# Performance work log

Hardware: AMD Instinct MI355X
Metric: run time of the kernel (lower is better)

## Reference

```python
import jax, jax.numpy as jnp
import numpy as np

H = 4096      # num_patches (sequence length)
WS = 8        # window_size
SHIFT = 4     # shift_size
NH = 8        # num_heads
DIM = 512     # embedding dim
HD = DIM // NH
NW = H // WS  # windows per batch element
B = 16
LN_EPS = 1e-5


def _layer_norm(x, g, b):
    m = jnp.mean(x, axis=-1, keepdims=True)
    v = jnp.var(x, axis=-1, keepdims=True)
    return (x - m) * jax.lax.rsqrt(v + LN_EPS) * g + b


def _window_partition(x):
    # Faithful to the repo: reshape->permute(nW<->ws)->flatten, giving strided windows.
    Bx, N, C = x.shape
    return x.reshape(Bx, N // WS, WS, C).transpose(0, 2, 1, 3).reshape(-1, WS, C)


def _window_reverse(w, N, Bx):
    C = w.shape[-1]
    return w.reshape(Bx, N // WS, WS, C).transpose(0, 2, 1, 3).reshape(Bx, N, C)


def _attn_mask():
    # Built exactly as in __init__ (numpy, constant at trace time): (NW, WS, WS)
    m = np.zeros((1, H, 1), np.float32)
    m[:, :H - WS] = 0.0
    m[:, H - WS:H - SHIFT] = 1.0
    m[:, H - SHIFT:] = 2.0
    mw = m.reshape(1, NW, WS, 1).transpose(0, 2, 1, 3).reshape(-1, WS)  # (NW, WS)
    d = mw[:, None, :] - mw[:, :, None]
    return np.where(d != 0, np.float32(-100.0), np.float32(0.0))


def _forward(x, norm1_g, norm1_b, qkv_w, qkv_b, proj_w, proj_b,
             norm2_g, norm2_b, fc1_w, fc1_b, fc2_w, fc2_b):
    Bx = x.shape[0]
    shortcut = x
    xn = _layer_norm(x, norm1_g, norm1_b)
    xs = jnp.roll(xn, -SHIFT, axis=1)
    xw = _window_partition(xs)                       # (Bx*NW, WS, DIM)
    B_ = xw.shape[0]
    qkv = xw @ qkv_w.T + qkv_b                       # (B_, WS, 3*DIM)
    qkv = qkv.reshape(B_, WS, 3, NH, HD).transpose(2, 0, 3, 1, 4)
    q, k, v = qkv[0], qkv[1], qkv[2]                 # (B_, NH, WS, HD)
    attn = jnp.einsum('bhqd,bhkd->bhqk', q, k) * (HD ** -0.5)
    mask = jnp.asarray(_attn_mask())                 # (NW, WS, WS)
    attn = attn.reshape(B_ // NW, NW, NH, WS, WS) + mask[None, :, None]
    attn = jax.nn.softmax(attn.reshape(B_, NH, WS, WS), axis=-1)
    o = jnp.einsum('bhqk,bhkd->bqhd', attn, v).reshape(B_, WS, DIM)
    o = o @ proj_w.T + proj_b
    xr = _window_reverse(o, H, Bx)
    xr = jnp.roll(xr, SHIFT, axis=1)
    x1 = shortcut + xr
    h = _layer_norm(x1, norm2_g, norm2_b)
    h = jax.nn.gelu(h @ fc1_w.T + fc1_b, approximate=False)
    h = h @ fc2_w.T + fc2_b
    return x1 + h


def setup_inputs() -> dict:
    key = jax.random.key(0)
    ks = jax.random.split(key, 8)
    s = 0.02
    return {
        'x': jax.random.normal(ks[0], (B, H, DIM), jnp.float32),
        'norm1_g': jnp.ones((DIM,), jnp.float32),
        'norm1_b': jnp.zeros((DIM,), jnp.float32),
        'qkv_w': jax.random.normal(ks[1], (3 * DIM, DIM), jnp.float32) * s,
        'qkv_b': jnp.zeros((3 * DIM,), jnp.float32),
        'proj_w': jax.random.normal(ks[2], (DIM, DIM), jnp.float32) * s,
        'proj_b': jnp.zeros((DIM,), jnp.float32),
        'norm2_g': jnp.ones((DIM,), jnp.float32),
        'norm2_b': jnp.zeros((DIM,), jnp.float32),
        'fc1_w': jax.random.normal(ks[3], (4 * DIM, DIM), jnp.float32) * s,
        'fc1_b': jnp.zeros((4 * DIM,), jnp.float32),
        'fc2_w': jax.random.normal(ks[4], (DIM, 4 * DIM), jnp.float32) * s,
        'fc2_b': jnp.zeros((DIM,), jnp.float32),
    }


def reference(x, norm1_g, norm1_b, qkv_w, qkv_b, proj_w, proj_b,
              norm2_g, norm2_b, fc1_w, fc1_b, fc2_w, fc2_b):
    return _forward(x, norm1_g, norm1_b, qkv_w, qkv_b, proj_w, proj_b,
                    norm2_g, norm2_b, fc1_w, fc1_b, fc2_w, fc2_b)
```

## Files before the change

kernel.cpp:

```cpp
#include <hip/hip_runtime.h>
#include <hip/hip_bf16.h>
#include <math.h>

typedef unsigned short ushortT;
typedef __attribute__((ext_vector_type(8))) short short8;
typedef __attribute__((ext_vector_type(4))) short short4v;
typedef __attribute__((ext_vector_type(4))) float f32x4;
typedef __attribute__((ext_vector_type(4))) float float4v;

#define TOK 65536
#define NSEQ 4096
#define DIM 512

__device__ __forceinline__ float bf2f(ushortT u) {
  union { float f; unsigned int i; } v; v.i = ((unsigned int)u) << 16; return v.f;
}
__device__ __forceinline__ ushortT f2bf(float f) {
  union { float f; unsigned int i; } v; v.f = f;
  unsigned int r = v.i + 0x7fffu + ((v.i >> 16) & 1u);
  return (ushortT)(r >> 16);
}

__device__ __forceinline__ float fast_gelu(float x) {
  const float y = fabsf(x) * 0.70710678118654752f;
  const float t = __builtin_amdgcn_rcpf(__builtin_fmaf(0.3275911f, y, 1.f));
  float p = 1.061405429f;
  p = __builtin_fmaf(p, t, -1.453152027f);
  p = __builtin_fmaf(p, t, 1.421413741f);
  p = __builtin_fmaf(p, t, -0.284496736f);
  p = __builtin_fmaf(p, t, 0.254829592f);
  p = p * t;
  const float e = __builtin_amdgcn_exp2f(-y * y * 1.4426950408889634f);
  float erfv = __builtin_fmaf(-p, e, 1.f);
  erfv = copysignf(erfv, x);
  return 0.5f * x * (1.f + erfv);
}

#define GLOAD_LDS(gp, lp) __builtin_amdgcn_global_load_lds( \
    (const __attribute__((address_space(1))) unsigned int*)(gp), \
    (__attribute__((address_space(3))) unsigned int*)(lp), 16, 0, 0)

#define LGKM0 do { asm volatile("s_waitcnt lgkmcnt(0)" ::: "memory"); \
                   __builtin_amdgcn_sched_barrier(0); } while (0)
#define BAR __builtin_amdgcn_s_barrier()
#define VMC(n) asm volatile("s_waitcnt vmcnt(" #n ")" ::: "memory")
#define SB0 __builtin_amdgcn_sched_barrier(0)

__global__ void cvt_kernel(const float* __restrict__ in, ushortT* __restrict__ out, int n4) {
  int i = blockIdx.x * 256 + threadIdx.x;
  if (i >= n4) return;
  float4v v = *(const float4v*)(in + (size_t)i * 4);
  short4v o;
#pragma unroll
  for (int j = 0; j < 4; ++j) o[j] = (short)f2bf(v[j]);
  *(short4v*)(out + (size_t)i * 4) = o;
}

template <bool INBF>
__global__ __launch_bounds__(256)
void ln_kernel(const void* __restrict__ inp, const float* __restrict__ gw,
               const float* __restrict__ bw, ushortT* __restrict__ out)
{
  const int lane = threadIdx.x & 63;
  const size_t tok = (size_t)blockIdx.x * 4 + (threadIdx.x >> 6);
  const int col = lane * 8;
  float x[8];
  if constexpr (INBF) {
    short8 v = *(const short8*)((const ushortT*)inp + tok * DIM + col);
#pragma unroll
    for (int j = 0; j < 8; ++j) x[j] = bf2f((ushortT)v[j]);
  } else {
    const float* p = (const float*)inp + tok * DIM + col;
    float4v a = *(const float4v*)p, b = *(const float4v*)(p + 4);
#pragma unroll
    for (int j = 0; j < 4; ++j) { x[j] = a[j]; x[4 + j] = b[j]; }
  }
  float s = 0.f, ss = 0.f;
#pragma unroll
  for (int j = 0; j < 8; ++j) { s += x[j]; ss += x[j] * x[j]; }
#pragma unroll
  for (int off = 1; off < 64; off <<= 1) {
    s += __shfl_xor(s, off, 64);
    ss += __shfl_xor(ss, off, 64);
  }
  const float mean = s * (1.f / 512.f);
  const float var = ss * (1.f / 512.f) - mean * mean;
  const float rstd = rsqrtf(var + 1e-5f);
  float4v g1 = *(const float4v*)(gw + col), g2 = *(const float4v*)(gw + col + 4);
  float4v b1 = *(const float4v*)(bw + col), b2 = *(const float4v*)(bw + col + 4);
  short8 o;
#pragma unroll
  for (int j = 0; j < 4; ++j) {
    o[j]     = (short)f2bf((x[j]     - mean) * rstd * g1[j] + b1[j]);
    o[4 + j] = (short)f2bf((x[4 + j] - mean) * rstd * g2[j] + b2[j]);
  }
  *(short8*)(out + tok * DIM + col) = o;
}

#define MFMA_PHASE(MQ, NQ) \
  _Pragma("unroll") \
  for (int s_ = 0; s_ < 2; ++s_) \
    _Pragma("unroll") \
    for (int m_ = 0; m_ < 4; ++m_) \
      _Pragma("unroll") \
      for (int n_ = 0; n_ < 2; ++n_) \
        acc[(MQ) * 4 + m_][(NQ) * 2 + n_] = __builtin_amdgcn_mfma_f32_16x16x32_bf16( \
            Af[m_][s_], Bf[NQ][n_][s_], acc[(MQ) * 4 + m_][(NQ) * 2 + n_], 0, 0, 0)

#define STAGE_A(bufp, h, kt) do { \
    GLOAD_LDS(gA + (size_t)((h) * 128) * K + (size_t)(kt) * 64,     (bufp) + (h) * 8192 + w * 1024); \
    GLOAD_LDS(gA + (size_t)((h) * 128 + 8) * K + (size_t)(kt) * 64, (bufp) + (h) * 8192 + w * 1024 + 512); \
  } while (0)
#define STAGE_B(bufp, h, kt) do { \
    GLOAD_LDS(gB + (size_t)((h) * 128) * K + (size_t)(kt) * 64,     (bufp) + (h) * 8192 + w * 1024); \
    GLOAD_LDS(gB + (size_t)((h) * 128 + 8) * K + (size_t)(kt) * 64, (bufp) + (h) * 8192 + w * 1024 + 512); \
  } while (0)

template <int EPI>
__global__ __launch_bounds__(512, 2)
void gemm256(const ushortT* __restrict__ A, const ushortT* __restrict__ Bt,
             const float* __restrict__ bias, int M, int N, int K,
             ushortT* __restrict__ outb, float* __restrict__ outf,
             const float* __restrict__ resf, const ushortT* __restrict__ resb)
{
  __shared__ __align__(16) ushortT sm[65536];
  ushortT* const Ab0 = sm;
  ushortT* const Ab1 = sm + 16384;
  ushortT* const Bb0 = sm + 32768;
  ushortT* const Bb1 = sm + 49152;

  const int tid = threadIdx.x;
  const int w = tid >> 6, l = tid & 63;
  const int wr = w >> 2, wc = w & 3;

  const int nwg = gridDim.x * gridDim.y;
  int wg = blockIdx.y * gridDim.x + blockIdx.x;
  {
    const int q = nwg >> 3, r8 = nwg & 7;
    const int xc = wg & 7, yc = wg >> 3;
    wg = (xc < r8 ? xc * (q + 1) : r8 * (q + 1) + (xc - r8) * q) + yc;
  }
  const int nbn = N >> 8;
  const int mb = wg / nbn, nb = wg % nbn;
  const int m0 = mb << 8, n0 = nb << 8;
  const int NT = K >> 6;

  const ushortT* gA = A  + (size_t)(m0 + w * 16 + (l >> 3)) * K + (((l & 7) ^ (l >> 3)) << 3);
  const ushortT* gB = Bt + (size_t)(n0 + w * 16 + (l >> 3)) * K + (((l & 7) ^ (l >> 3)) << 3);

  const int rl = l & 15, ql = l >> 4;
  const int aoff = (wr * 128 + rl) * 64;
  const int boff = (wc * 64 + rl) * 64;
  const int cs0 = ((ql) ^ (l & 7)) << 3;
  const int cs1 = ((4 + ql) ^ (l & 7)) << 3;

  f32x4 acc[8][4];
  const f32x4 zero = {0.f, 0.f, 0.f, 0.f};
#pragma unroll
  for (int i = 0; i < 8; ++i)
#pragma unroll
    for (int j = 0; j < 4; ++j) acc[i][j] = zero;

  ushortT* Ac = Ab0; ushortT* An = Ab1;
  ushortT* Bc = Bb0; ushortT* Bn = Bb1;

  STAGE_A(Ac, 0, 0); STAGE_A(Ac, 1, 0); STAGE_B(Bc, 0, 0); STAGE_B(Bc, 1, 0);
  STAGE_A(An, 0, 1); STAGE_A(An, 1, 1); STAGE_B(Bn, 0, 1);
  VMC(6);
  BAR;

  short8 Af[4][2];
  short8 Bf[2][2][2];

  for (int t = 0; t < NT; ++t) {
#pragma unroll
    for (int m = 0; m < 4; ++m) {
      Af[m][0] = *(const short8*)(Ac + aoff + m * 1024 + cs0);
      Af[m][1] = *(const short8*)(Ac + aoff + m * 1024 + cs1);
    }
#pragma unroll
    for (int n = 0; n < 2; ++n) {
      Bf[0][n][0] = *(const short8*)(Bc + boff + n * 1024 + cs0);
      Bf[0][n][1] = *(const short8*)(Bc + boff + n * 1024 + cs1);
    }
    if (t + 1 < NT) STAGE_B(Bn, 1, t + 1);
    SB0;
    BAR; LGKM0;
    __builtin_amdgcn_s_setprio(1);
    MFMA_PHASE(0, 0);
    __builtin_amdgcn_s_setprio(0);
    BAR;
#pragma unroll
    for (int n = 0; n < 2; ++n) {
      Bf[1][n][0] = *(const short8*)(Bc + boff + (2 + n) * 1024 + cs0);
      Bf[1][n][1] = *(const short8*)(Bc + boff + (2 + n) * 1024 + cs1);
    }
    SB0;
    BAR; LGKM0;
    __builtin_amdgcn_s_setprio(1);
    MFMA_PHASE(0, 1);
    __builtin_amdgcn_s_setprio(0);
    BAR;
#pragma unroll
    for (int m = 0; m < 4; ++m) {
      Af[m][0] = *(const short8*)(Ac + aoff + (4 + m) * 1024 + cs0);
      Af[m][1] = *(const short8*)(Ac + aoff + (4 + m) * 1024 + cs1);
    }
    SB0;
    BAR; LGKM0;
    __builtin_amdgcn_s_setprio(1);
    MFMA_PHASE(1, 0);
    __builtin_amdgcn_s_setprio(0);
    BAR;
    SB0;
    if (t + 2 < NT) {
      STAGE_A(Ac, 0, t + 2); STAGE_A(Ac, 1, t + 2); STAGE_B(Bc, 0, t + 2);
      VMC(6);
    } else if (t + 1 < NT) {
      VMC(0);
    }
    __builtin_amdgcn_s_setprio(1);
    MFMA_PHASE(1, 1);
    __builtin_amdgcn_s_setprio(0);
    BAR;
    ushortT* tp;
    tp = Ac; Ac = An; An = tp;
    tp = Bc; Bc = Bn; Bn = tp;
  }

#pragma unroll
  for (int m = 0; m < 8; ++m) {
#pragma unroll
    for (int n = 0; n < 4; ++n) {
      const int col = n0 + wc * 64 + n * 16 + rl;
      const float bb = bias[col];
#pragma unroll
      for (int i = 0; i < 4; ++i) {
        const size_t row = (size_t)(m0 + wr * 128 + m * 16 + ql * 4 + i);
        float v = acc[m][n][i] + bb;
        if constexpr (EPI == 1) v += resf[row * (size_t)N + col];
        if constexpr (EPI == 2) v = fast_gelu(v);
        if constexpr (EPI == 3) {
          v += bf2f(resb[row * (size_t)N + col]);
          outf[row * (size_t)N + col] = v;
        } else {
          outb[row * (size_t)N + col] = f2bf(v);
        }
      }
    }
  }
}

__global__ __launch_bounds__(512)
void attn_kernel(const ushortT* __restrict__ qkv, ushortT* __restrict__ out)
{
  __shared__ __align__(16) ushortT sq[8][1544];
  const int wb = blockIdx.x;
  const int b  = wb >> 9;
  const int rr = wb & 511;
  const int w1 = rr >> 6;
  const int g  = rr & 63;
  const int tid = threadIdx.x;

#pragma unroll
  for (int c = 0; c < 3; ++c) {
    const int f = c * 512 + tid;
    const int i = f / 192;
    const int col = (f % 192) * 8;
    const int tin = (64 * g + 8 * i + w1 + 4) & (NSEQ - 1);
    const ushortT* src = qkv + ((size_t)b * NSEQ + tin) * 1536 + col;
    *(short8*)(&sq[i][col]) = *(const short8*)src;
  }
  __syncthreads();

  const int wave = tid >> 6, lane = tid & 63;
  const int h = wave;
  const int qi = lane >> 3, kj = lane & 7;

  float s = 0.f;
  const ushortT* qrow = &sq[qi][h * 64];
  const ushortT* krow = &sq[kj][512 + h * 64];
#pragma unroll
  for (int c = 0; c < 8; ++c) {
    short8 qa = *(const short8*)(qrow + c * 8);
    short8 ka = *(const short8*)(krow + c * 8);
#pragma unroll
    for (int j = 0; j < 8; ++j) s += bf2f((ushortT)qa[j]) * bf2f((ushortT)ka[j]);
  }
  s *= 0.125f;

  const int pq = 64 * g + 8 * qi + w1;
  const int pk = 64 * g + 8 * kj + w1;
  const int cq = (pq < 4088) ? 0 : (pq < 4092 ? 1 : 2);
  const int ck = (pk < 4088) ? 0 : (pk < 4092 ? 1 : 2);
  if (cq != ck) s -= 100.f;

  float mx = s;
  mx = fmaxf(mx, __shfl_xor(mx, 1, 64));
  mx = fmaxf(mx, __shfl_xor(mx, 2, 64));
  mx = fmaxf(mx, __shfl_xor(mx, 4, 64));
  const float e = expf(s - mx);
  float sum = e;
  sum += __shfl_xor(sum, 1, 64);
  sum += __shfl_xor(sum, 2, 64);
  sum += __shfl_xor(sum, 4, 64);
  const float p = e / sum;

  const int dc = lane & 7;
  float o[8];
#pragma unroll
  for (int j = 0; j < 8; ++j) o[j] = 0.f;
#pragma unroll
  for (int k2 = 0; k2 < 8; ++k2) {
    const float pk2 = __shfl(p, (lane & ~7) + k2, 64);
    short8 va = *(const short8*)(&sq[k2][1024 + h * 64 + dc * 8]);
#pragma unroll
    for (int j = 0; j < 8; ++j) o[j] += pk2 * bf2f((ushortT)va[j]);
  }

  const int tout = (512 * qi + 64 * w1 + g + 4) & (NSEQ - 1);
  short8 ov;
#pragma unroll
  for (int j = 0; j < 8; ++j) ov[j] = (short)f2bf(o[j]);
  *(short8*)(out + ((size_t)b * NSEQ + tout) * DIM + h * 64 + dc * 8) = ov;
}

extern "C" void kernel_launch(void* const* d_in, const int* in_sizes, int n_in,
                              void* d_out, int out_size, void* d_ws, size_t ws_size,
                              hipStream_t stream) {
  const float* x      = (const float*)d_in[0];
  const float* n1g    = (const float*)d_in[1];
  const float* n1b    = (const float*)d_in[2];
  const float* qkv_w  = (const float*)d_in[3];
  const float* qkv_b  = (const float*)d_in[4];
  const float* proj_w = (const float*)d_in[5];
  const float* proj_b = (const float*)d_in[6];
  const float* n2g    = (const float*)d_in[7];
  const float* n2b    = (const float*)d_in[8];
  const float* fc1_w  = (const float*)d_in[9];
  const float* fc1_b  = (const float*)d_in[10];
  const float* fc2_w  = (const float*)d_in[11];
  const float* fc2_b  = (const float*)d_in[12];
  float* out = (float*)d_out;

  size_t off = 0;
  char* ws = (char*)d_ws;
  auto alloc = [&](size_t b) { void* p = ws + off; off += (b + 255) & ~(size_t)255; return p; };

  ushortT* qkvw_b = (ushortT*)alloc((size_t)1536 * 512 * 2);
  ushortT* projw_b = (ushortT*)alloc((size_t)512 * 512 * 2);
  ushortT* fc1w_b = (ushortT*)alloc((size_t)2048 * 512 * 2);
  ushortT* fc2w_b = (ushortT*)alloc((size_t)512 * 2048 * 2);
  ushortT* bufA = (ushortT*)alloc((size_t)TOK * 512 * 2);
  ushortT* bufQ = (ushortT*)alloc((size_t)TOK * 1536 * 2);
  ushortT* x1 = bufQ;

  int nch = 1;
  while (nch < 16) {
    size_t need = (size_t)(TOK / nch) * 2048 * 2;
    if (off + need <= ws_size) break;
    nch <<= 1;
  }
  ushortT* h1 = (ushortT*)(ws + off);

  cvt_kernel<<<(1536 * 512 / 4 + 255) / 256, 256, 0, stream>>>(qkv_w, qkvw_b, 1536 * 512 / 4);
  cvt_kernel<<<(512 * 512 / 4 + 255) / 256, 256, 0, stream>>>(proj_w, projw_b, 512 * 512 / 4);
  cvt_kernel<<<(2048 * 512 / 4 + 255) / 256, 256, 0, stream>>>(fc1_w, fc1w_b, 2048 * 512 / 4);
  cvt_kernel<<<(512 * 2048 / 4 + 255) / 256, 256, 0, stream>>>(fc2_w, fc2w_b, 512 * 2048 / 4);

  ln_kernel<false><<<TOK / 4, 256, 0, stream>>>(x, n1g, n1b, bufA);

  gemm256<0><<<dim3(TOK / 256, 1536 / 256), 512, 0, stream>>>(
      bufA, qkvw_b, qkv_b, TOK, 1536, 512, bufQ, nullptr, nullptr, nullptr);

  attn_kernel<<<8192, 512, 0, stream>>>(bufQ, bufA);

  gemm256<1><<<dim3(TOK / 256, 512 / 256), 512, 0, stream>>>(
      bufA, projw_b, proj_b, TOK, 512, 512, x1, nullptr, x, nullptr);

  ln_kernel<true><<<TOK / 4, 256, 0, stream>>>(x1, n2g, n2b, bufA);

  const int tc = TOK / nch;
  for (int c = 0; c < nch; ++c) {
    const ushortT* hin = bufA + (size_t)c * tc * 512;
    gemm256<2><<<dim3(tc / 256, 2048 / 256), 512, 0, stream>>>(
        hin, fc1w_b, fc1_b, tc, 2048, 512, h1, nullptr, nullptr, nullptr);
    gemm256<3><<<dim3(tc / 256, 512 / 256), 512, 0, stream>>>(
        h1, fc2w_b, fc2_b, tc, 512, 2048, nullptr, out + (size_t)c * tc * 512,
        nullptr, x1 + (size_t)c * tc * 512);
  }
}
```

Baseline: 700.0 us.

## Restructure GEMM main loop to simple double-buffered prefetch with k-split fragment phases

Replaces the staggered two-tile-ahead staging scheme with a plain double buffer. The whole next k-tile is issued at the start of each iteration and waited on at the end. The MFMA phases are reorganised to split along the k-halves (cs0/cs1) with all four B fragments live, rather than splitting along N. This removes some barriers and register-held fragment arrays, which simplifies scheduling and lowers register pressure. In exchange, load latency is hidden by only one iteration of compute instead of the finer-grained interleaving.

```diff
diff --git a/kernel.cpp b/kernel.cpp
--- a/kernel.cpp
+++ b/kernel.cpp
@@ -97,23 +97,21 @@
   *(short8*)(out + tok * DIM + col) = o;
 }
 
-#define MFMA_PHASE(MQ, NQ) \
+#define MFMA_PHASE(MH) \
   _Pragma("unroll") \
-  for (int s_ = 0; s_ < 2; ++s_) \
+  for (int m_ = 0; m_ < 4; ++m_) \
     _Pragma("unroll") \
-    for (int m_ = 0; m_ < 4; ++m_) \
-      _Pragma("unroll") \
-      for (int n_ = 0; n_ < 2; ++n_) \
-        acc[(MQ) * 4 + m_][(NQ) * 2 + n_] = __builtin_amdgcn_mfma_f32_16x16x32_bf16( \
-            Af[m_][s_], Bf[NQ][n_][s_], acc[(MQ) * 4 + m_][(NQ) * 2 + n_], 0, 0, 0)
-
-#define STAGE_A(bufp, h, kt) do { \
-    GLOAD_LDS(gA + (size_t)((h) * 128) * K + (size_t)(kt) * 64,     (bufp) + (h) * 8192 + w * 1024); \
-    GLOAD_LDS(gA + (size_t)((h) * 128 + 8) * K + (size_t)(kt) * 64, (bufp) + (h) * 8192 + w * 1024 + 512); \
+    for (int n_ = 0; n_ < 4; ++n_) \
+      acc[(MH) * 4 + m_][n_] = __builtin_amdgcn_mfma_f32_16x16x32_bf16( \
+          Af[m_], Bf[n_], acc[(MH) * 4 + m_][n_], 0, 0, 0)
+
+#define STAGE_A2(bufp, h, gptr) do { \
+    GLOAD_LDS((gptr) + (size_t)((h) * 128) * K,     (bufp) + (h) * 8192 + w * 1024); \
+    GLOAD_LDS((gptr) + (size_t)((h) * 128 + 8) * K, (bufp) + (h) * 8192 + w * 1024 + 512); \
   } while (0)
-#define STAGE_B(bufp, h, kt) do { \
-    GLOAD_LDS(gB + (size_t)((h) * 128) * K + (size_t)(kt) * 64,     (bufp) + (h) * 8192 + w * 1024); \
-    GLOAD_LDS(gB + (size_t)((h) * 128 + 8) * K + (size_t)(kt) * 64, (bufp) + (h) * 8192 + w * 1024 + 512); \
+#define STAGE_B2(bufp, h, gptr) do { \
+    GLOAD_LDS((gptr) + (size_t)((h) * 128) * K,     (bufp) + (h) * 8192 + w * 1024); \
+    GLOAD_LDS((gptr) + (size_t)((h) * 128 + 8) * K, (bufp) + (h) * 8192 + w * 1024 + 512); \
   } while (0)
 
 template <int EPI>
@@ -164,68 +162,53 @@
   ushortT* Ac = Ab0; ushortT* An = Ab1;
   ushortT* Bc = Bb0; ushortT* Bn = Bb1;
 
-  STAGE_A(Ac, 0, 0); STAGE_A(Ac, 1, 0); STAGE_B(Bc, 0, 0); STAGE_B(Bc, 1, 0);
-  STAGE_A(An, 0, 1); STAGE_A(An, 1, 1); STAGE_B(Bn, 0, 1);
-  VMC(6);
+  STAGE_A2(Ac, 0, gA); STAGE_A2(Ac, 1, gA);
+  STAGE_B2(Bc, 0, gB); STAGE_B2(Bc, 1, gB);
+  VMC(0);
   BAR;
 
-  short8 Af[4][2];
-  short8 Bf[2][2][2];
+  short8 Af[4], Bf[4];
+  size_t koff = 64;
 
   for (int t = 0; t < NT; ++t) {
 #pragma unroll
-    for (int m = 0; m < 4; ++m) {
-      Af[m][0] = *(const short8*)(Ac + aoff + m * 1024 + cs0);
-      Af[m][1] = *(const short8*)(Ac + aoff + m * 1024 + cs1);
+    for (int m = 0; m < 4; ++m) Af[m] = *(const short8*)(Ac + aoff + m * 1024 + cs0);
+#pragma unroll
+    for (int n = 0; n < 4; ++n) Bf[n] = *(const short8*)(Bc + boff + n * 1024 + cs0);
+    if (t + 1 < NT) {
+      STAGE_A2(An, 0, gA + koff); STAGE_A2(An, 1, gA + koff);
+      STAGE_B2(Bn, 0, gB + koff); STAGE_B2(Bn, 1, gB + koff);
     }
-#pragma unroll
-    for (int n = 0; n < 2; ++n) {
-      Bf[0][n][0] = *(const short8*)(Bc + boff + n * 1024 + cs0);
-      Bf[0][n][1] = *(const short8*)(Bc + boff + n * 1024 + cs1);
-    }
-    if (t + 1 < NT) STAGE_B(Bn, 1, t + 1);
-    SB0;
-    BAR; LGKM0;
+    SB0; BAR; LGKM0;
     __builtin_amdgcn_s_setprio(1);
-    MFMA_PHASE(0, 0);
+    MFMA_PHASE(0);
     __builtin_amdgcn_s_setprio(0);
-    BAR;
-#pragma unroll
-    for (int n = 0; n < 2; ++n) {
-      Bf[1][n][0] = *(const short8*)(Bc + boff + (2 + n) * 1024 + cs0);
-      Bf[1][n][1] = *(const short8*)(Bc + boff + (2 + n) * 1024 + cs1);
-    }
-    SB0;
-    BAR; LGKM0;
+#pragma unroll
+    for (int m = 0; m < 4; ++m) Af[m] = *(const short8*)(Ac + aoff + (4 + m) * 1024 + cs0);
+    SB0; BAR; LGKM0;
     __builtin_amdgcn_s_setprio(1);
-    MFMA_PHASE(0, 1);
+    MFMA_PHASE(1);
     __builtin_amdgcn_s_setprio(0);
-    BAR;
-#pragma unroll
-    for (int m = 0; m < 4; ++m) {
-      Af[m][0] = *(const short8*)(Ac + aoff + (4 + m) * 1024 + cs0);
-      Af[m][1] = *(const short8*)(Ac + aoff + (4 + m) * 1024 + cs1);
-    }
-    SB0;
-    BAR; LGKM0;
+#pragma unroll
+    for (int m = 0; m < 4; ++m) Af[m] = *(const short8*)(Ac + aoff + m * 1024 + cs1);
+#pragma unroll
+    for (int n = 0; n < 4; ++n) Bf[n] = *(const short8*)(Bc + boff + n * 1024 + cs1);
+    SB0; BAR; LGKM0;
     __builtin_amdgcn_s_setprio(1);
-    MFMA_PHASE(1, 0);
+    MFMA_PHASE(0);
     __builtin_amdgcn_s_setprio(0);
-    BAR;
-    SB0;
-    if (t + 2 < NT) {
-      STAGE_A(Ac, 0, t + 2); STAGE_A(Ac, 1, t + 2); STAGE_B(Bc, 0, t + 2);
-      VMC(6);
-    } else if (t + 1 < NT) {
-      VMC(0);
-    }
+#pragma unroll
+    for (int m = 0; m < 4; ++m) Af[m] = *(const short8*)(Ac + aoff + (4 + m) * 1024 + cs1);
+    SB0; BAR; LGKM0;
     __builtin_amdgcn_s_setprio(1);
-    MFMA_PHASE(1, 1);
+    MFMA_PHASE(1);
     __builtin_amdgcn_s_setprio(0);
+    if (t + 1 < NT) VMC(0);
     BAR;
     ushortT* tp;
     tp = Ac; Ac = An; An = tp;
     tp = Bc; Bc = Bn; Bn = tp;
+    koff += 64;
   }
 
 #pragma unroll
```

New measurement: 706.5 us, median of 2. About the same (+0.9%).
